# Optimization experiments

Hardware: AMD Instinct MI355X
Metric: run time of the kernel (lower is better)

The kernel has to match this reference:

```python
import jax, jax.numpy as jnp
import numpy as np

NUM_HEADS = 8
EPS = 1e-8

def setup_inputs() -> dict:
    key = jax.random.key(0)
    k1, k2, k3 = jax.random.split(key, 3)
    batch, L, dim = 2, 2048, 512
    B = jax.random.normal(k1, (batch, L, dim), dtype=jnp.float32)
    C = jax.random.normal(k2, (batch, L, dim), dtype=jnp.float32)
    S = jax.random.uniform(k3, (batch, L, dim), dtype=jnp.float32)
    return {"B": B, "C": C, "S": S}

def reference(B, C, S):
    batch, L, dim = B.shape
    H = NUM_HEADS
    d = dim // H
    # [b, H, L, d]
    Bh = B.reshape(batch, L, H, d).transpose(0, 2, 1, 3)
    Ch = C.reshape(batch, L, H, d).transpose(0, 2, 1, 3)
    Ah = S.reshape(batch, L, H, d).transpose(0, 2, 1, 3)
    # cum_A[0] = 1, cum_A[i] = prod_{k=1..i} A_k  (matches torch loop)
    cum_A = jnp.cumprod(Ah.at[:, :, 0, :].set(1.0), axis=2)
    ones = jnp.ones_like(cum_A[:, :, :1])
    # P[i] = cum_A[i-1] (P[0]=1): numerator of the product between j and i
    P = jnp.concatenate([ones, cum_A[:, :, :-1]], axis=2)
    # D[j] = cum_A[j-1] + eps for j>=1, D[0]=1 (j==0 branch has no eps)
    D = jnp.concatenate([ones, cum_A[:, :, :-1] + EPS], axis=2)
    # T_ij = sum_d C_i P_i B_j / D_j   for j < i
    T = jnp.einsum('bhid,bhjd->bhij', Ch * P, Bh / D)
    diag_vals = jnp.sum(Ch * Bh, axis=-1)  # T_ii = C_i . B_i
    idx = jnp.arange(L)
    strict_lower = idx[:, None] > idx[None, :]
    T = jnp.where(strict_lower, T, 0.0)
    T = T + diag_vals[:, :, :, None] * jnp.eye(L, dtype=T.dtype)
    # causal masking of strict upper triangle is already zero; use_softmax=False
    return T
```

## Files before the change

### kernel.cpp

```cpp
#include <hip/hip_runtime.h>
#include <hip/hip_bf16.h>

#define LL   2048
#define DIM  512
#define HD   64
#define BHN  16
#define NC   128
#define CH   16
#define GC   8
#define EPSF 1e-8f

typedef __attribute__((ext_vector_type(8))) short bf16x8;
typedef __attribute__((ext_vector_type(4))) float f32x4;

__device__ __forceinline__ void nt_store(float* p, float v) {
    __builtin_nontemporal_store(v, p);
}
__device__ __forceinline__ void nt_store4(f32x4* p, f32x4 v) {
    __builtin_nontemporal_store(v, p);
}

__global__ __launch_bounds__(64) void chunkprod_kernel(const float* __restrict__ S,
                                                       float* __restrict__ U) {
    int c = blockIdx.x, bh = blockIdx.y;
    int b = bh >> 3, h = bh & 7;
    int d = threadIdx.x;
    int l0 = c * CH;
    size_t base = ((size_t)b * LL + l0) * DIM + h * HD + d;
    float p = 1.0f;
    #pragma unroll
    for (int l = 0; l < CH; ++l) {
        float a = S[base + (size_t)l * DIM];
        if (l0 + l >= 1) p *= a;
    }
    U[((size_t)bh * NC + c) * HD + d] = p;
}

__global__ __launch_bounds__(1024) void chunkscan_kernel(const float* __restrict__ U,
                                                         float* __restrict__ St) {
    int bh = blockIdx.x;
    int t = threadIdx.x;
    int g = t >> 6, d = t & 63;
    int c0 = g * GC;
    float u[GC];
    float prod = 1.0f;
    #pragma unroll
    for (int k = 0; k < GC; ++k) {
        u[k] = U[((size_t)bh * NC + c0 + k) * HD + d];
        prod *= u[k];
    }
    __shared__ float Ls[16][64];
    Ls[g][d] = prod;
    __syncthreads();
    float run = 1.0f;
    for (int gg = 0; gg < g; ++gg) run *= Ls[gg][d];
    #pragma unroll
    for (int k = 0; k < GC; ++k) {
        St[((size_t)bh * NC + c0 + k) * HD + d] = run;
        run *= u[k];
    }
}

__global__ __launch_bounds__(256) void diag_kernel(const float* __restrict__ Bg,
                                                   const float* __restrict__ Cg,
                                                   float* __restrict__ diag) {
    int w = threadIdx.x >> 6, lane = threadIdx.x & 63;
    int flat = blockIdx.x * 4 + w;
    int bh = flat >> 11, l = flat & (LL - 1);
    int b = bh >> 3, h = bh & 7;
    size_t gi = ((size_t)b * LL + l) * DIM + h * HD + lane;
    float tsum = Cg[gi] * Bg[gi];
    #pragma unroll
    for (int off = 1; off < 64; off <<= 1) tsum += __shfl_xor(tsum, off);
    if (lane == 0) diag[(size_t)bh * LL + l] = tsum;
}

__global__ __launch_bounds__(64) void apply_kernel(const float* __restrict__ Bg,
                                                   const float* __restrict__ Cg,
                                                   const float* __restrict__ S,
                                                   const float* __restrict__ St,
                                                   __hip_bfloat16* __restrict__ X,
                                                   __hip_bfloat16* __restrict__ Y) {
    int c = blockIdx.x, bh = blockIdx.y;
    int b = bh >> 3, h = bh & 7;
    int d = threadIdx.x;
    int l0 = c * CH;
    size_t gbase = ((size_t)b * LL + l0) * DIM + h * HD + d;
    float p = St[((size_t)bh * NC + c) * HD + d];
    #pragma unroll
    for (int l = 0; l < CH; ++l) {
        int gl = l0 + l;
        size_t gi = gbase + (size_t)l * DIM;
        float a = S[gi], bv = Bg[gi], cv = Cg[gi];
        float Dv = (gl == 0) ? 1.0f : (p + EPSF);
        size_t o = ((size_t)bh * LL + gl) * HD + d;
        X[o] = __float2bfloat16(cv * p);
        Y[o] = __float2bfloat16(bv / Dv);
        if (gl >= 1) p *= a;
    }
}

__global__ __launch_bounds__(256) void gemm_kernel(const __hip_bfloat16* __restrict__ X,
                                                   const __hip_bfloat16* __restrict__ Y,
                                                   const float* __restrict__ diag,
                                                   float* __restrict__ out) {
    int tj = blockIdx.x, ti = blockIdx.y, bh = blockIdx.z;
    size_t obase = (size_t)bh * LL * LL;
    int i0 = ti * 128, j0 = tj * 128;
    int t = threadIdx.x;

    if (tj > ti) {
        f32x4 z = {0.f, 0.f, 0.f, 0.f};
        int col4 = t & 31, row0 = t >> 5;
        float* ob = out + obase + (size_t)i0 * LL + j0;
        #pragma unroll
        for (int r = 0; r < 16; ++r)
            nt_store4((f32x4*)(ob + (size_t)(row0 + 8 * r) * LL) + col4, z);
        return;
    }

    __shared__ short Xs[128 * 64];
    __shared__ short Ys[128 * 64];

    {
        const f32x4* Xg4 = (const f32x4*)(X + ((size_t)bh * LL + i0) * HD);
        const f32x4* Yg4 = (const f32x4*)(Y + ((size_t)bh * LL + j0) * HD);
        int chunk = t & 7, r0 = t >> 3;
        int sc = (chunk ^ (r0 & 7)) * 8;
        #pragma unroll
        for (int p = 0; p < 4; ++p) {
            int row = r0 + 32 * p;
            f32x4 vx = Xg4[row * 8 + chunk];
            f32x4 vy = Yg4[row * 8 + chunk];
            *(f32x4*)&Xs[row * 64 + sc] = vx;
            *(f32x4*)&Ys[row * 64 + sc] = vy;
        }
    }
    __syncthreads();

    int lane = t & 63, wv = t >> 6;
    int wi = wv >> 1, wj = wv & 1;
    int l15 = lane & 15, q = lane >> 4;

    f32x4 acc[4][4] = {};
    #pragma unroll
    for (int kc = 0; kc < 2; ++kc) {
        bf16x8 af[4], bf[4];
        #pragma unroll
        for (int mt = 0; mt < 4; ++mt) {
            int row = 64 * wi + 16 * mt + l15;
            int sc = ((4 * kc + q) ^ (row & 7)) * 8;
            af[mt] = *(const bf16x8*)&Xs[row * 64 + sc];
        }
        #pragma unroll
        for (int nt = 0; nt < 4; ++nt) {
            int row = 64 * wj + 16 * nt + l15;
            int sc = ((4 * kc + q) ^ (row & 7)) * 8;
            bf[nt] = *(const bf16x8*)&Ys[row * 64 + sc];
        }
        #pragma unroll
        for (int mt = 0; mt < 4; ++mt)
            #pragma unroll
            for (int nt = 0; nt < 4; ++nt)
                acc[mt][nt] = __builtin_amdgcn_mfma_f32_16x16x32_bf16(
                    af[mt], bf[nt], acc[mt][nt], 0, 0, 0);
    }

    int i_base = i0 + 64 * wi, j_base = j0 + 64 * wj;
    if (tj < ti) {
        #pragma unroll
        for (int mt = 0; mt < 4; ++mt)
            #pragma unroll
            for (int reg = 0; reg < 4; ++reg) {
                int gi = i_base + 16 * mt + 4 * q + reg;
                float* ob = out + obase + (size_t)gi * LL + j_base;
                #pragma unroll
                for (int nt = 0; nt < 4; ++nt)
                    nt_store(ob + 16 * nt + l15, acc[mt][nt][reg]);
            }
    } else {
        #pragma unroll
        for (int mt = 0; mt < 4; ++mt)
            #pragma unroll
            for (int reg = 0; reg < 4; ++reg) {
                int gi = i_base + 16 * mt + 4 * q + reg;
                float dv = diag[(size_t)bh * LL + gi];
                float* ob = out + obase + (size_t)gi * LL + j_base;
                #pragma unroll
                for (int nt = 0; nt < 4; ++nt) {
                    int gj = j_base + 16 * nt + l15;
                    float v = acc[mt][nt][reg];
                    nt_store(ob + 16 * nt + l15,
                             (gj < gi) ? v : ((gj == gi) ? dv : 0.f));
                }
            }
    }
}

extern "C" void kernel_launch(void* const* d_in, const int* in_sizes, int n_in,
                              void* d_out, int out_size, void* d_ws, size_t ws_size,
                              hipStream_t stream) {
    const float* Bg = (const float*)d_in[0];
    const float* Cg = (const float*)d_in[1];
    const float* S  = (const float*)d_in[2];
    float* out = (float*)d_out;

    char* ws = (char*)d_ws;
    size_t xy_bytes = (size_t)BHN * LL * HD * sizeof(__hip_bfloat16);
    __hip_bfloat16* X = (__hip_bfloat16*)(ws);
    __hip_bfloat16* Y = (__hip_bfloat16*)(ws + xy_bytes);
    float* diag = (float*)(ws + 2 * xy_bytes);
    float* U    = (float*)(ws + 2 * xy_bytes + (size_t)BHN * LL * sizeof(float));
    float* St   = (float*)(ws + 2 * xy_bytes + (size_t)BHN * LL * sizeof(float)
                              + (size_t)BHN * NC * HD * sizeof(float));

    chunkprod_kernel<<<dim3(NC, BHN), 64, 0, stream>>>(S, U);
    chunkscan_kernel<<<BHN, 1024, 0, stream>>>(U, St);
    diag_kernel<<<(LL * BHN) / 4, 256, 0, stream>>>(Bg, Cg, diag);
    apply_kernel<<<dim3(NC, BHN), 64, 0, stream>>>(Bg, Cg, S, St, X, Y);
    gemm_kernel<<<dim3(16, 16, BHN), 256, 0, stream>>>(X, Y, diag, out);
}
```

Before: 304.6 us.

## Fold chunk scan and diagonal dot product into apply kernel

```diff
diff --git a/kernel.cpp b/kernel.cpp
--- a/kernel.cpp
+++ b/kernel.cpp
@@ -7,7 +7,6 @@
 #define BHN  16
 #define NC   128
 #define CH   16
-#define GC   8
 #define EPSF 1e-8f
 
 typedef __attribute__((ext_vector_type(8))) short bf16x8;
@@ -36,57 +35,24 @@
     U[((size_t)bh * NC + c) * HD + d] = p;
 }
 
-__global__ __launch_bounds__(1024) void chunkscan_kernel(const float* __restrict__ U,
-                                                         float* __restrict__ St) {
-    int bh = blockIdx.x;
-    int t = threadIdx.x;
-    int g = t >> 6, d = t & 63;
-    int c0 = g * GC;
-    float u[GC];
-    float prod = 1.0f;
-    #pragma unroll
-    for (int k = 0; k < GC; ++k) {
-        u[k] = U[((size_t)bh * NC + c0 + k) * HD + d];
-        prod *= u[k];
-    }
-    __shared__ float Ls[16][64];
-    Ls[g][d] = prod;
-    __syncthreads();
-    float run = 1.0f;
-    for (int gg = 0; gg < g; ++gg) run *= Ls[gg][d];
-    #pragma unroll
-    for (int k = 0; k < GC; ++k) {
-        St[((size_t)bh * NC + c0 + k) * HD + d] = run;
-        run *= u[k];
-    }
-}
-
-__global__ __launch_bounds__(256) void diag_kernel(const float* __restrict__ Bg,
-                                                   const float* __restrict__ Cg,
-                                                   float* __restrict__ diag) {
-    int w = threadIdx.x >> 6, lane = threadIdx.x & 63;
-    int flat = blockIdx.x * 4 + w;
-    int bh = flat >> 11, l = flat & (LL - 1);
-    int b = bh >> 3, h = bh & 7;
-    size_t gi = ((size_t)b * LL + l) * DIM + h * HD + lane;
-    float tsum = Cg[gi] * Bg[gi];
-    #pragma unroll
-    for (int off = 1; off < 64; off <<= 1) tsum += __shfl_xor(tsum, off);
-    if (lane == 0) diag[(size_t)bh * LL + l] = tsum;
-}
-
 __global__ __launch_bounds__(64) void apply_kernel(const float* __restrict__ Bg,
                                                    const float* __restrict__ Cg,
                                                    const float* __restrict__ S,
-                                                   const float* __restrict__ St,
+                                                   const float* __restrict__ U,
                                                    __hip_bfloat16* __restrict__ X,
-                                                   __hip_bfloat16* __restrict__ Y) {
+                                                   __hip_bfloat16* __restrict__ Y,
+                                                   float* __restrict__ diag) {
     int c = blockIdx.x, bh = blockIdx.y;
     int b = bh >> 3, h = bh & 7;
     int d = threadIdx.x;
     int l0 = c * CH;
+
+    float p = 1.0f;
+    for (int cc = 0; cc < c; ++cc)
+        p *= U[((size_t)bh * NC + cc) * HD + d];
+
     size_t gbase = ((size_t)b * LL + l0) * DIM + h * HD + d;
-    float p = St[((size_t)bh * NC + c) * HD + d];
+    float tv[CH];
     #pragma unroll
     for (int l = 0; l < CH; ++l) {
         int gl = l0 + l;
@@ -96,7 +62,23 @@
         size_t o = ((size_t)bh * LL + gl) * HD + d;
         X[o] = __float2bfloat16(cv * p);
         Y[o] = __float2bfloat16(bv / Dv);
+        tv[l] = cv * bv;
         if (gl >= 1) p *= a;
+    }
+    #pragma unroll
+    for (int l = 0; l < CH; ++l) {
+        float s = tv[l];
+        #pragma unroll
+        for (int off = 1; off < 64; off <<= 1) s += __shfl_xor(s, off);
+        tv[l] = s;
+    }
+    if (d == 0) {
+        float* dp = diag + (size_t)bh * LL + l0;
+        #pragma unroll
+        for (int q4 = 0; q4 < CH / 4; ++q4) {
+            f32x4 v = {tv[4 * q4], tv[4 * q4 + 1], tv[4 * q4 + 2], tv[4 * q4 + 3]};
+            *((f32x4*)dp + q4) = v;
+        }
     }
 }
 
@@ -211,12 +193,8 @@
     __hip_bfloat16* Y = (__hip_bfloat16*)(ws + xy_bytes);
     float* diag = (float*)(ws + 2 * xy_bytes);
     float* U    = (float*)(ws + 2 * xy_bytes + (size_t)BHN * LL * sizeof(float));
-    float* St   = (float*)(ws + 2 * xy_bytes + (size_t)BHN * LL * sizeof(float)
-                              + (size_t)BHN * NC * HD * sizeof(float));
 
     chunkprod_kernel<<<dim3(NC, BHN), 64, 0, stream>>>(S, U);
-    chunkscan_kernel<<<BHN, 1024, 0, stream>>>(U, St);
-    diag_kernel<<<(LL * BHN) / 4, 256, 0, stream>>>(Bg, Cg, diag);
-    apply_kernel<<<dim3(NC, BHN), 64, 0, stream>>>(Bg, Cg, S, St, X, Y);
+    apply_kernel<<<dim3(NC, BHN), 64, 0, stream>>>(Bg, Cg, S, U, X, Y, diag);
     gemm_kernel<<<dim3(16, 16, BHN), 256, 0, stream>>>(X, Y, diag, out);
 }
```

Measured after the change: 323.7 us. +6.3%, slower.
